# Optimization experiments

Hardware: AMD Instinct MI355X
Metric: run time of the kernel (lower is better)

## Reference

```python
import jax, jax.numpy as jnp
import numpy as np
import math

L, E, H, T, B, V = 6, 768, 12, 1024, 4, 256
HS = E // H


def _ln(x, w, b, eps=1e-5):
    mu = jnp.mean(x, axis=-1, keepdims=True)
    var = jnp.mean((x - mu) ** 2, axis=-1, keepdims=True)
    return (x - mu) * jax.lax.rsqrt(var + eps) * w + b


def setup_inputs() -> dict:
    key = jax.random.key(0)
    ks = jax.random.split(key, 12)
    std = 0.02
    inp = {
        "idx": jax.random.randint(ks[0], (B, T), 0, V, dtype=jnp.int64),
        "tok_emb": jax.random.normal(ks[1], (V, E), jnp.float32) * std,
        "pos_emb": jnp.zeros((1, T, E), jnp.float32),
        "ln1_w": jnp.ones((L, E), jnp.float32),
        "ln1_b": jnp.zeros((L, E), jnp.float32),
        "Wq": jax.random.normal(ks[2], (L, E, E), jnp.float32) * std,
        "bq": jnp.zeros((L, E), jnp.float32),
        "Wk": jax.random.normal(ks[3], (L, E, E), jnp.float32) * std,
        "bk": jnp.zeros((L, E), jnp.float32),
        "Wv": jax.random.normal(ks[4], (L, E, E), jnp.float32) * std,
        "bv": jnp.zeros((L, E), jnp.float32),
        "Wp": jax.random.normal(ks[5], (L, E, E), jnp.float32) * std,
        "bp": jnp.zeros((L, E), jnp.float32),
        "ln2_w": jnp.ones((L, E), jnp.float32),
        "ln2_b": jnp.zeros((L, E), jnp.float32),
        "W1": jax.random.normal(ks[6], (L, E, 4 * E), jnp.float32) * std,
        "b1": jnp.zeros((L, 4 * E), jnp.float32),
        "W2": jax.random.normal(ks[7], (L, 4 * E, E), jnp.float32) * std,
        "b2": jnp.zeros((L, E), jnp.float32),
        "lnf_w": jnp.ones((E,), jnp.float32),
        "lnf_b": jnp.zeros((E,), jnp.float32),
        "lm_head": jax.random.normal(ks[8], (E, V), jnp.float32) * std,
    }
    return inp


def reference(idx, tok_emb, pos_emb, ln1_w, ln1_b, Wq, bq, Wk, bk, Wv, bv, Wp, bp,
              ln2_w, ln2_b, W1, b1, W2, b2, lnf_w, lnf_b, lm_head):
    Bc, Tc = idx.shape
    causal = jnp.tril(jnp.ones((Tc, Tc), bool))  # [T,T]
    scale = 1.0 / math.sqrt(HS)
    x = tok_emb[idx] + pos_emb[:, :Tc, :]  # [B,T,E]
    for l in range(L):
        h = _ln(x, ln1_w[l], ln1_b[l])
        q = (h @ Wq[l] + bq[l]).reshape(Bc, Tc, H, HS).transpose(0, 2, 1, 3)
        k = (h @ Wk[l] + bk[l]).reshape(Bc, Tc, H, HS).transpose(0, 2, 1, 3)
        v = (h @ Wv[l] + bv[l]).reshape(Bc, Tc, H, HS).transpose(0, 2, 1, 3)
        att = jnp.einsum('bhtd,bhsd->bhts', q, k) * scale  # [B,H,T,T]
        att = jnp.where(causal, att, -jnp.inf)
        att = jax.nn.softmax(att, axis=-1)
        y = jnp.einsum('bhts,bhsd->bhtd', att, v)
        y = y.transpose(0, 2, 1, 3).reshape(Bc, Tc, E)
        x = x + (y @ Wp[l] + bp[l])
        h2 = _ln(x, ln2_w[l], ln2_b[l])
        m = jax.nn.gelu(h2 @ W1[l] + b1[l], approximate=False)
        x = x + (m @ W2[l] + b2[l])
    x = _ln(x, lnf_w, lnf_b)
    logits = x @ lm_head  # [B,T,V]
    return logits
```

## Files before the change

kernel.cpp:

```cpp
#include <hip/hip_runtime.h>

#define L_ 6
#define E_ 768
#define H_ 12
#define T_ 1024
#define B_ 4
#define V_ 256
#define M_ (B_*T_)
#define E4_ (4*E_)
#define QKVN (3*E_)
#define NZP 2
#define NZL 4

typedef __bf16 bf16;
typedef __bf16 bf16x8 __attribute__((ext_vector_type(8)));
typedef __bf16 bf16x4 __attribute__((ext_vector_type(4)));
typedef float f32x4 __attribute__((ext_vector_type(4)));

#define GF_GELU     1
#define GF_BIAS_EXT 16
#define GF_PART     32

__device__ __forceinline__ float ldf(const void* p, size_t i, int f32m) {
    return f32m ? ((const float*)p)[i] : (float)((const bf16*)p)[i];
}

__device__ __forceinline__ void async_cp16(const void* g, void* l) {
    __builtin_amdgcn_global_load_lds(
        (__attribute__((address_space(1))) void*)g,
        (__attribute__((address_space(3))) void*)l, 16, 0, 0);
}

__device__ __forceinline__ float exp2_hw(float x) {
    float r; asm("v_exp_f32 %0, %1" : "=v"(r) : "v"(x)); return r;
}

__device__ __forceinline__ float gelu_f(float v) {
    float ax = fabsf(v) * 0.70710678118654752f;
    float t  = 1.f / (1.f + 0.3275911f * ax);
    float p  = t*(0.254829592f + t*(-0.284496736f + t*(1.421413741f
             + t*(-1.453152027f + t*1.061405429f))));
    float e  = exp2_hw(-1.4426950408889634f * ax * ax);
    float er = __builtin_copysignf(1.f - p * e, v);
    return 0.5f * v * (1.f + er);
}

__global__ __launch_bounds__(256) void k_probe(const void* __restrict__ tok,
    const void* __restrict__ idxp, int* __restrict__ dm)
{
    __shared__ int sc1, sc2;
    if (threadIdx.x == 0) { sc1 = 0; sc2 = 0; }
    __syncthreads();
    const bf16* tb = (const bf16*)tok;
    int c1 = 0;
    for (int i = threadIdx.x; i < 4096; i += 256) {
        float v = (float)tb[2 * i];
        if (!(fabsf(v) < 100.f)) c1++;
    }
    const int* ip = (const int*)idxp;
    int c2 = 0;
    for (int i = threadIdx.x; i < 1024; i += 256)
        if (ip[2 * i + 1] != 0) c2++;
    atomicAdd(&sc1, c1);
    atomicAdd(&sc2, c2);
    __syncthreads();
    if (threadIdx.x == 0) { dm[0] = (sc1 > 400) ? 1 : 0; dm[1] = (sc2 < 100) ? 1 : 0; }
}

__global__ __launch_bounds__(256) void k_embed(const void* __restrict__ idxp,
    const void* __restrict__ tok, const void* __restrict__ pos,
    float* __restrict__ x, const int* __restrict__ dm)
{
    int f32m = dm[0], i64m = dm[1];
    int bt = blockIdx.x;
    int t  = bt & (T_ - 1);
    int id = i64m ? ((const int*)idxp)[2 * bt] : ((const int*)idxp)[bt];
    float* xo = x + (size_t)bt * E_;
    for (int e = threadIdx.x; e < E_; e += 256)
        xo[e] = ldf(tok, (size_t)id * E_ + e, f32m) + ldf(pos, (size_t)t * E_ + e, f32m);
}

__global__ __launch_bounds__(256) void k_ln(const float* __restrict__ x,
    const void* __restrict__ w, const void* __restrict__ b, size_t wboff,
    bf16* __restrict__ out, const int* __restrict__ dm)
{
    int f32m = dm[0];
    int row = blockIdx.x;
    int tid = threadIdx.x;
    const float* xr = x + (size_t)row * E_;
    float v0 = xr[tid], v1 = xr[tid + 256], v2 = xr[tid + 512];
    float s  = v0 + v1 + v2;
    float s2 = v0*v0 + v1*v1 + v2*v2;
    for (int off = 32; off; off >>= 1) {
        s  += __shfl_xor(s,  off);
        s2 += __shfl_xor(s2, off);
    }
    __shared__ float ls[4], ls2[4];
    int wave = tid >> 6;
    if ((tid & 63) == 0) { ls[wave] = s; ls2[wave] = s2; }
    __syncthreads();
    s  = ls[0] + ls[1] + ls[2] + ls[3];
    s2 = ls2[0] + ls2[1] + ls2[2] + ls2[3];
    float mu  = s * (1.0f / E_);
    float var = s2 * (1.0f / E_) - mu * mu;
    float rs  = rsqrtf(var + 1e-5f);
    bf16* o = out + (size_t)row * E_;
    o[tid]       = (bf16)(((v0 - mu) * rs) * ldf(w, wboff + tid,       f32m) + ldf(b, wboff + tid,       f32m));
    o[tid + 256] = (bf16)(((v1 - mu) * rs) * ldf(w, wboff + tid + 256, f32m) + ldf(b, wboff + tid + 256, f32m));
    o[tid + 512] = (bf16)(((v2 - mu) * rs) * ldf(w, wboff + tid + 512, f32m) + ldf(b, wboff + tid + 512, f32m));
}

__global__ __launch_bounds__(256) void k_red_ln(float* __restrict__ x,
    const float* __restrict__ part,
    const void* __restrict__ gb, size_t gboff,
    const void* __restrict__ w, const void* __restrict__ b, size_t wboff,
    bf16* __restrict__ out, const int* __restrict__ dm)
{
    const size_t PSTR = (size_t)M_ * E_;
    int f32m = dm[0];
    int row = blockIdx.x;
    int tid = threadIdx.x;
    float* xr = x + (size_t)row * E_;
    const float* pr = part + (size_t)row * E_;
    float v[3];
    #pragma unroll
    for (int j = 0; j < 3; j++) {
        int c = tid + j * 256;
        float acc = xr[c];
        #pragma unroll
        for (int z = 0; z < NZP; z++) acc += pr[(size_t)z * PSTR + c];
        acc += ldf(gb, gboff + c, f32m);
        v[j] = acc;
        xr[c] = acc;
    }
    float s  = v[0] + v[1] + v[2];
    float s2 = v[0]*v[0] + v[1]*v[1] + v[2]*v[2];
    for (int off = 32; off; off >>= 1) {
        s  += __shfl_xor(s,  off);
        s2 += __shfl_xor(s2, off);
    }
    __shared__ float ls[4], ls2[4];
    int wave = tid >> 6;
    if ((tid & 63) == 0) { ls[wave] = s; ls2[wave] = s2; }
    __syncthreads();
    s  = ls[0] + ls[1] + ls[2] + ls[3];
    s2 = ls2[0] + ls2[1] + ls2[2] + ls2[3];
    float mu  = s * (1.0f / E_);
    float var = s2 * (1.0f / E_) - mu * mu;
    float rs  = rsqrtf(var + 1e-5f);
    bf16* o = out + (size_t)row * E_;
    #pragma unroll
    for (int j = 0; j < 3; j++) {
        int c = tid + j * 256;
        o[c] = (bf16)(((v[j] - mu) * rs) * ldf(w, wboff + c, f32m) + ldf(b, wboff + c, f32m));
    }
}

__global__ __launch_bounds__(256) void k_transposeZ(const void* __restrict__ in,
    size_t inoff, size_t zin, bf16* __restrict__ out, size_t zout,
    int R, int C, const int* __restrict__ dm)
{
    int f32m = dm[0];
    __shared__ bf16 tile[32][33];
    size_t io = inoff + (size_t)blockIdx.z * zin;
    bf16* o = out + (size_t)blockIdx.z * zout;
    int r0 = blockIdx.x * 32, c0 = blockIdx.y * 32;
    int tx = threadIdx.x & 31, ty = threadIdx.x >> 5;
    #pragma unroll
    for (int i = 0; i < 4; i++)
        tile[ty + 8*i][tx] = (bf16)ldf(in, io + (size_t)(r0 + ty + 8*i) * C + (c0 + tx), f32m);
    __syncthreads();
    #pragma unroll
    for (int i = 0; i < 4; i++)
        o[(size_t)(c0 + ty + 8*i) * R + (r0 + tx)] = tile[tx][ty + 8*i];
}

__global__ __launch_bounds__(256) void k_transpose3L(const void* __restrict__ a,
    const void* __restrict__ b, const void* __restrict__ c,
    bf16* __restrict__ out, const int* __restrict__ dm)
{
    int f32m = dm[0];
    int z = blockIdx.z, l = z / 3, wsel = z - 3 * l;
    const void* in = (wsel == 0) ? a : ((wsel == 1) ? b : c);
    size_t io = (size_t)l * E_ * E_;
    bf16* o = out + (size_t)z * E_ * E_;
    __shared__ bf16 tile[32][33];
    int r0 = blockIdx.x * 32, c0 = blockIdx.y * 32;
    int tx = threadIdx.x & 31, ty = threadIdx.x >> 5;
    #pragma unroll
    for (int i = 0; i < 4; i++)
        tile[ty + 8*i][tx] = (bf16)ldf(in, io + (size_t)(r0 + ty + 8*i) * E_ + (c0 + tx), f32m);
    __syncthreads();
    #pragma unroll
    for (int i = 0; i < 4; i++)
        o[(size_t)(c0 + ty + 8*i) * E_ + (r0 + tx)] = tile[tx][ty + 8*i];
}

__global__ __launch_bounds__(256) void k_cat3L(const void* __restrict__ a,
    const void* __restrict__ b, const void* __restrict__ c,
    bf16* __restrict__ o, const int* __restrict__ dm)
{
    int f32m = dm[0];
    int i = blockIdx.x * 256 + threadIdx.x;
    int l = i / QKVN, j = i - l * QKVN;
    float v = (j < E_) ? ldf(a, (size_t)l * E_ + j, f32m)
            : ((j < 2*E_) ? ldf(b, (size_t)l * E_ + j - E_, f32m)
                          : ldf(c, (size_t)l * E_ + j - 2*E_, f32m));
    o[i] = (bf16)v;
}

__global__ __launch_bounds__(256) void k_cast_red(const float* __restrict__ in,
    void* __restrict__ out, const int* __restrict__ dm)
{
    const size_t S = (size_t)M_ * V_ / 4;
    size_t i = (size_t)blockIdx.x * 256 + threadIdx.x;
    const f32x4* p = (const f32x4*)in;
    f32x4 v = p[i];
    v += p[S + i];
    v += p[2*S + i];
    v += p[3*S + i];
    if (dm[0]) {
        ((f32x4*)out)[i] = v;
    } else {
        bf16x4 o;
        #pragma unroll
        for (int j = 0; j < 4; j++) o[j] = (bf16)v[j];
        ((bf16x4*)out)[i] = o;
    }
}

__global__ __launch_bounds__(256) void k_gemm(const bf16* __restrict__ A,
    const bf16* __restrict__ BT, const void* __restrict__ bias, size_t boff,
    void* __restrict__ outp, int M, int N, int K, int flags, const int* __restrict__ dm)
{
    int f32m = dm[0];
    __shared__ __attribute__((aligned(16))) bf16 As[128 * 64];
    __shared__ __attribute__((aligned(16))) bf16 Bs[128 * 64];
    int tid = threadIdx.x;
    int bn0 = blockIdx.x * 128, bm0 = blockIdx.y * 128;
    int kz = blockIdx.z;
    int Ks = K / gridDim.z;
    int kbeg = kz * Ks, kend = kbeg + Ks;
    int wave = tid >> 6, lane = tid & 63, quad = lane >> 4, l16 = lane & 15;
    int wr = wave >> 1, wc = wave & 1;

    int st_col = 8 * ((lane & 7) ^ (lane >> 3));
    int st_row_base = wave * 32 + (lane >> 3);

    f32x4 acc[4][4];
    #pragma unroll
    for (int i = 0; i < 4; i++)
        #pragma unroll
        for (int j = 0; j < 4; j++)
            acc[i][j] = (f32x4){0.f, 0.f, 0.f, 0.f};

    int sw = l16 & 7;
    for (int k0 = kbeg; k0 < kend; k0 += 64) {
        #pragma unroll
        for (int i = 0; i < 4; i++) {
            int row = st_row_base + i * 8;
            const bf16* ga = A  + (size_t)(bm0 + row) * K + k0 + st_col;
            const bf16* gb = BT + (size_t)(bn0 + row) * K + k0 + st_col;
            bf16* la = As + (size_t)(wave * 256 + i * 64) * 8;
            bf16* lb = Bs + (size_t)(wave * 256 + i * 64) * 8;
            async_cp16(ga, la);
            async_cp16(gb, lb);
        }
        __syncthreads();
        #pragma unroll
        for (int ks = 0; ks < 2; ks++) {
            bf16x8 af[4], bfr[4];
            #pragma unroll
            for (int mi = 0; mi < 4; mi++) {
                int row = wr*64 + mi*16 + l16;
                int kgs = (4*ks + quad) ^ sw;
                af[mi] = *(const bf16x8*)&As[row*64 + kgs*8];
            }
            #pragma unroll
            for (int ni = 0; ni < 4; ni++) {
                int row = wc*64 + ni*16 + l16;
                int kgs = (4*ks + quad) ^ sw;
                bfr[ni] = *(const bf16x8*)&Bs[row*64 + kgs*8];
            }
            #pragma unroll
            for (int mi = 0; mi < 4; mi++)
                #pragma unroll
                for (int ni = 0; ni < 4; ni++)
                    acc[mi][ni] = __builtin_amdgcn_mfma_f32_16x16x32_bf16(af[mi], bfr[ni], acc[mi][ni], 0, 0, 0);
        }
        __syncthreads();
    }

    float* pout = (float*)outp + (size_t)kz * M * N;
    #pragma unroll
    for (int mi = 0; mi < 4; mi++) {
        #pragma unroll
        for (int ni = 0; ni < 4; ni++) {
            int col = bn0 + wc*64 + ni*16 + l16;
            float bv = 0.f;
            if (bias)
                bv = (flags & GF_BIAS_EXT) ? ldf(bias, boff + col, f32m)
                                           : (float)((const bf16*)bias)[col];
            #pragma unroll
            for (int r = 0; r < 4; r++) {
                int row = bm0 + wr*64 + mi*16 + quad*4 + r;
                float val = acc[mi][ni][r] + bv;
                if (flags & GF_GELU) val = gelu_f(val);
                size_t oidx = (size_t)row * N + col;
                if (flags & GF_PART) pout[oidx] = val;
                else                 ((bf16*)outp)[oidx] = (bf16)val;
            }
        }
    }
}

__global__ __launch_bounds__(256) void k_gemm64(const bf16* __restrict__ A,
    const bf16* __restrict__ BT, void* __restrict__ outp,
    int M, int N, int K, int flags, const int* __restrict__ dm)
{
    __shared__ __attribute__((aligned(16))) bf16 As[128 * 64];
    __shared__ __attribute__((aligned(16))) bf16 Bs[64 * 64];
    int tid = threadIdx.x;
    int bn0 = blockIdx.x * 64, bm0 = blockIdx.y * 128;
    int kz = blockIdx.z;
    int Ks = K / gridDim.z;
    int kbeg = kz * Ks, kend = kbeg + Ks;
    int wave = tid >> 6, lane = tid & 63, quad = lane >> 4, l16 = lane & 15;
    int wr = wave >> 1, wc = wave & 1;

    int st_col = 8 * ((lane & 7) ^ (lane >> 3));
    int lrow = lane >> 3;

    f32x4 acc[4][2];
    #pragma unroll
    for (int i = 0; i < 4; i++)
        #pragma unroll
        for (int j = 0; j < 2; j++)
            acc[i][j] = (f32x4){0.f, 0.f, 0.f, 0.f};

    int sw = l16 & 7;
    for (int k0 = kbeg; k0 < kend; k0 += 64) {
        #pragma unroll
        for (int i = 0; i < 4; i++) {
            int row = wave * 32 + i * 8 + lrow;
            async_cp16(A + (size_t)(bm0 + row) * K + k0 + st_col,
                       As + (size_t)(wave * 32 + i * 8) * 64);
        }
        #pragma unroll
        for (int i = 0; i < 2; i++) {
            int row = wave * 16 + i * 8 + lrow;
            async_cp16(BT + (size_t)(bn0 + row) * K + k0 + st_col,
                       Bs + (size_t)(wave * 16 + i * 8) * 64);
        }
        __syncthreads();
        #pragma unroll
        for (int ks = 0; ks < 2; ks++) {
            int kgs = (4*ks + quad) ^ sw;
            bf16x8 af[4], bfr[2];
            #pragma unroll
            for (int mi = 0; mi < 4; mi++)
                af[mi] = *(const bf16x8*)&As[(wr*64 + mi*16 + l16)*64 + kgs*8];
            #pragma unroll
            for (int ni = 0; ni < 2; ni++)
                bfr[ni] = *(const bf16x8*)&Bs[(wc*32 + ni*16 + l16)*64 + kgs*8];
            #pragma unroll
            for (int mi = 0; mi < 4; mi++)
                #pragma unroll
                for (int ni = 0; ni < 2; ni++)
                    acc[mi][ni] = __builtin_amdgcn_mfma_f32_16x16x32_bf16(af[mi], bfr[ni], acc[mi][ni], 0, 0, 0);
        }
        __syncthreads();
    }

    float* pout = (float*)outp + (size_t)kz * M * N;
    #pragma unroll
    for (int mi = 0; mi < 4; mi++) {
        #pragma unroll
        for (int ni = 0; ni < 2; ni++) {
            int col = bn0 + wc*32 + ni*16 + l16;
            #pragma unroll
            for (int r = 0; r < 4; r++) {
                int row = bm0 + wr*64 + mi*16 + quad*4 + r;
                float val = acc[mi][ni][r];
                size_t oidx = (size_t)row * N + col;
                if (flags & GF_PART) pout[oidx] = val;
                else                 ((bf16*)outp)[oidx] = (bf16)val;
            }
        }
    }
}

__device__ __forceinline__ void attn_qk_softmax2(
    const bf16x8 qf[2], f32x4 OT[4], float& m_ln, float& l_ln,
    const bf16* __restrict__ Kbuf, bf16 (*Ps)[72],
    int wave, int quad, int l16, int s0, int qt0, bool diag)
{
    f32x4 S[4];
    #pragma unroll
    for (int i = 0; i < 4; i++) S[i] = (f32x4){0.f, 0.f, 0.f, 0.f};
    #pragma unroll
    for (int ks = 0; ks < 2; ks++)
        #pragma unroll
        for (int ni = 0; ni < 4; ni++) {
            int kg = (ks*4 + quad) ^ (l16 & 7);
            bf16x8 kf = *(const bf16x8*)&Kbuf[(ni*16 + l16)*64 + kg*8];
            S[ni] = __builtin_amdgcn_mfma_f32_16x16x32_bf16(kf, qf[ks], S[ni], 0, 0, 0);
        }
    const float SC = 0.18033688011112042f;
    if (diag) {
        int qr = qt0 + wave*16 + l16;
        #pragma unroll
        for (int ni = 0; ni < 4; ni++)
            #pragma unroll
            for (int r = 0; r < 4; r++) {
                int scol = s0 + ni*16 + quad*4 + r;
                S[ni][r] = (scol > qr) ? -1e30f : S[ni][r] * SC;
            }
    } else {
        #pragma unroll
        for (int ni = 0; ni < 4; ni++)
            #pragma unroll
            for (int r = 0; r < 4; r++) S[ni][r] *= SC;
    }
    float tn[4];
    #pragma unroll
    for (int ni = 0; ni < 4; ni++)
        tn[ni] = fmaxf(fmaxf(S[ni][0], S[ni][1]), fmaxf(S[ni][2], S[ni][3]));
    float tm = fmaxf(fmaxf(tn[0], tn[1]), fmaxf(tn[2], tn[3]));
    tm = fmaxf(tm, __shfl_xor(tm, 16));
    tm = fmaxf(tm, __shfl_xor(tm, 32));
    float mnew = fmaxf(m_ln, tm);
    float alpha = exp2_hw(m_ln - mnew);
    m_ln = mnew;
    float rsum = 0.f;
    bf16x4 pk[4];
    #pragma unroll
    for (int ni = 0; ni < 4; ni++)
        #pragma unroll
        for (int r = 0; r < 4; r++) {
            float p = exp2_hw(S[ni][r] - mnew);
            rsum += p;
            pk[ni][r] = (bf16)p;
        }
    rsum += __shfl_xor(rsum, 16);
    rsum += __shfl_xor(rsum, 32);
    l_ln = l_ln * alpha + rsum;
    #pragma unroll
    for (int ni = 0; ni < 4; ni++)
        #pragma unroll
        for (int r = 0; r < 4; r++) OT[ni][r] *= alpha;
    #pragma unroll
    for (int ni = 0; ni < 4; ni++)
        *(bf16x4*)&Ps[wave*16 + l16][ni*16 + quad*4] = pk[ni];
}

__device__ __forceinline__ void attn_pv(
    f32x4 OT[4], const bf16 (*Ps)[72], const bf16 (*Vt)[72],
    int wave, int quad, int l16)
{
    #pragma unroll
    for (int ks = 0; ks < 2; ks++) {
        bf16x8 pf = *(const bf16x8*)&Ps[wave*16 + l16][ks*32 + quad*8];
        #pragma unroll
        for (int ni = 0; ni < 4; ni++) {
            bf16x8 vf = *(const bf16x8*)&Vt[ni*16 + l16][ks*32 + quad*8];
            OT[ni] = __builtin_amdgcn_mfma_f32_16x16x32_bf16(vf, pf, OT[ni], 0, 0, 0);
        }
    }
}

__global__ __launch_bounds__(256) void k_attn(const bf16* __restrict__ qkv, bf16* __restrict__ y)
{
    int x = blockIdx.x;
    int qt = x * 64;
    int h = blockIdx.y, b = blockIdx.z;
    int tid = threadIdx.x, wave = tid >> 6, lane = tid & 63, quad = lane >> 4, l16 = lane & 15;

    const bf16* qb = qkv + (size_t)b * T_ * QKVN + h * 64;
    const bf16* kb = qb + E_;
    const bf16* vb = qb + 2 * E_;

    __shared__ __attribute__((aligned(16))) bf16 Kbuf[64 * 64];
    __shared__ __attribute__((aligned(16))) bf16 Vbuf[64 * 64];
    __shared__ __attribute__((aligned(16))) bf16 Vt[64][72];
    __shared__ __attribute__((aligned(16))) bf16 Ps[64][72];

    int srow = tid >> 3;
    int scol = 8 * ((lane & 7) ^ (srow & 7));

    bf16x8 qf[2];
    {
        int qr = qt + wave * 16 + l16;
        #pragma unroll
        for (int ks = 0; ks < 2; ks++)
            qf[ks] = *(const bf16x8*)(qb + (size_t)qr * QKVN + ks*32 + quad*8);
    }

    f32x4 OT[4];
    #pragma unroll
    for (int i = 0; i < 4; i++) OT[i] = (f32x4){0.f,0.f,0.f,0.f};
    float m_ln = -3.0e38f, l_ln = 0.f;

    auto stage = [&](int s0) {
        #pragma unroll
        for (int i = 0; i < 2; i++) {
            int row = i * 32 + srow;
            const bf16* gk = kb + (size_t)(s0 + row) * QKVN + scol;
            const bf16* gv = vb + (size_t)(s0 + row) * QKVN + scol;
            bf16* lk = Kbuf + ((size_t)i * 32 + wave * 8) * 64;
            bf16* lv = Vbuf + ((size_t)i * 32 + wave * 8) * 64;
            async_cp16(gk, lk);
            async_cp16(gv, lv);
        }
    };

    stage(0);
    asm volatile("s_waitcnt vmcnt(0)" ::: "memory");
    __syncthreads();

    for (int st = 0; st <= x; st++) {
        int s0 = st * 64;
        {
            int d = lane;
            int dg = d >> 3, de = d & 7;
            #pragma unroll
            for (int ii = 0; ii < 2; ii++) {
                int sb = wave * 2 + ii;
                bf16x8 tv;
                #pragma unroll
                for (int j = 0; j < 8; j++)
                    tv[j] = Vbuf[(sb*8 + j) * 64 + ((dg ^ j) * 8) + de];
                *(bf16x8*)&Vt[d][sb * 8] = tv;
            }
        }
        attn_qk_softmax2(qf, OT, m_ln, l_ln, Kbuf, Ps, wave, quad, l16, s0, qt, st == x);
        __syncthreads();
        if (st < x) stage(s0 + 64);
        attn_pv(OT, Ps, Vt, wave, quad, l16);
        asm volatile("s_waitcnt vmcnt(0)" ::: "memory");
        __syncthreads();
    }

    float inv = 1.f / l_ln;
    int qrow = qt + wave * 16 + l16;
    #pragma unroll
    for (int ni = 0; ni < 4; ni++) {
        bf16x4 ov;
        #pragma unroll
        for (int r = 0; r < 4; r++) ov[r] = (bf16)(OT[ni][r] * inv);
        *(bf16x4*)&y[(size_t)(b * T_ + qrow) * E_ + h*64 + ni*16 + quad*4] = ov;
    }
}

extern "C" void kernel_launch(void* const* d_in, const int* in_sizes, int n_in,
                              void* d_out, int out_size, void* d_ws, size_t ws_size,
                              hipStream_t stream)
{
    const void* idx     = d_in[0];
    const void* tok_emb = d_in[1];
    const void* pos_emb = d_in[2];
    const void* ln1_w   = d_in[3];
    const void* ln1_b   = d_in[4];
    const void* Wq      = d_in[5];
    const void* bq      = d_in[6];
    const void* Wk      = d_in[7];
    const void* bk      = d_in[8];
    const void* Wv      = d_in[9];
    const void* bv      = d_in[10];
    const void* Wp      = d_in[11];
    const void* bp      = d_in[12];
    const void* ln2_w   = d_in[13];
    const void* ln2_b   = d_in[14];
    const void* W1      = d_in[15];
    const void* b1      = d_in[16];
    const void* W2      = d_in[17];
    const void* b2      = d_in[18];
    const void* lnf_w   = d_in[19];
    const void* lnf_b   = d_in[20];
    const void* lm_head = d_in[21];

    char* base = (char*)d_ws;
    size_t off = 0;
    auto nxt = [&](size_t bytes) -> void* {
        void* p = base + off;
        off += (bytes + 255) & ~(size_t)255;
        return p;
    };
    int*   dm    = (int*)  nxt(256);
    float* x     = (float*)nxt((size_t)M_ * E_ * 4);
    bf16*  h     = (bf16*) nxt((size_t)M_ * E_ * 2);
    bf16*  qkv   = (bf16*) nxt((size_t)M_ * QKVN * 2);
    bf16*  yb    = (bf16*) nxt((size_t)M_ * E_ * 2);
    bf16*  mbuf  = (bf16*) nxt((size_t)M_ * E4_ * 2);
    bf16*  wqkvT = (bf16*) nxt((size_t)L_ * 3 * E_ * E_ * 2);
    bf16*  wpT   = (bf16*) nxt((size_t)L_ * E_ * E_ * 2);
    bf16*  w1T   = (bf16*) nxt((size_t)L_ * E_ * E4_ * 2);
    bf16*  w2T   = (bf16*) nxt((size_t)L_ * E4_ * E_ * 2);
    bf16*  lmhT  = (bf16*) nxt((size_t)V_ * E_ * 2);
    bf16*  bcat  = (bf16*) nxt((size_t)L_ * QKVN * 2);
    float* part  = (float*)nxt((size_t)NZL * M_ * V_ * 4 > (size_t)NZP * M_ * E_ * 4
                             ? (size_t)NZL * M_ * V_ * 4 : (size_t)NZP * M_ * E_ * 4);
    (void)ws_size; (void)in_sizes; (void)n_in; (void)out_size;

    k_probe<<<1, 256, 0, stream>>>(tok_emb, idx, dm);
    k_embed<<<M_, 256, 0, stream>>>(idx, tok_emb, pos_emb, x, dm);

    k_transpose3L<<<dim3(E_/32, E_/32, 3*L_), 256, 0, stream>>>(Wq, Wk, Wv, wqkvT, dm);
    k_transposeZ<<<dim3(E_/32, E_/32, L_), 256, 0, stream>>>(Wp, 0, (size_t)E_*E_, wpT, (size_t)E_*E_, E_, E_, dm);
    k_transposeZ<<<dim3(E_/32, E4_/32, L_), 256, 0, stream>>>(W1, 0, (size_t)E_*E4_, w1T, (size_t)E_*E4_, E_, E4_, dm);
    k_transposeZ<<<dim3(E4_/32, E_/32, L_), 256, 0, stream>>>(W2, 0, (size_t)E_*E4_, w2T, (size_t)E_*E4_, E4_, E_, dm);
    k_transposeZ<<<dim3(E_/32, V_/32, 1), 256, 0, stream>>>(lm_head, 0, 0, lmhT, 0, E_, V_, dm);
    k_cat3L<<<(L_*QKVN)/256, 256, 0, stream>>>(bq, bk, bv, bcat, dm);

    k_ln<<<M_, 256, 0, stream>>>(x, ln1_w, ln1_b, 0, h, dm);

    for (int l = 0; l < L_; l++) {
        size_t voE  = (size_t)l * E_;
        size_t voE4 = (size_t)l * E4_;

        k_gemm<<<dim3(QKVN/128, M_/128), 256, 0, stream>>>(h, wqkvT + (size_t)l*3*E_*E_,
            bcat + (size_t)l*QKVN, 0, qkv, M_, QKVN, E_, 0, dm);

        k_attn<<<dim3(16, H_, B_), 256, 0, stream>>>(qkv, yb);

        k_gemm64<<<dim3(E_/64, M_/128, NZP), 256, 0, stream>>>(yb, wpT + (size_t)l*E_*E_,
            part, M_, E_, E_, GF_PART, dm);
        k_red_ln<<<M_, 256, 0, stream>>>(x, part, bp, voE, ln2_w, ln2_b, voE, h, dm);

        k_gemm<<<dim3(E4_/128, M_/128), 256, 0, stream>>>(h, w1T + (size_t)l*E_*E4_,
            b1, voE4, mbuf, M_, E4_, E_, GF_GELU | GF_BIAS_EXT, dm);

        k_gemm64<<<dim3(E_/64, M_/128, NZP), 256, 0, stream>>>(mbuf, w2T + (size_t)l*E_*E4_,
            part, M_, E_, E4_, GF_PART, dm);
        if (l < L_ - 1)
            k_red_ln<<<M_, 256, 0, stream>>>(x, part, b2, voE, ln1_w, ln1_b, (size_t)(l+1) * E_, h, dm);
        else
            k_red_ln<<<M_, 256, 0, stream>>>(x, part, b2, voE, lnf_w, lnf_b, 0, h, dm);
    }

    k_gemm64<<<dim3(V_/64, M_/128, NZL), 256, 0, stream>>>(h, lmhT, part, M_, V_, E_, GF_PART, dm);
    k_cast_red<<<(M_*V_)/1024, 256, 0, stream>>>(part, d_out, dm);
}
```

Before: 1.366 ms.

## Double-buffer GEMM LDS tiles and fuse residual add into projection epilogues

Both GEMM kernels now keep two LDS buffers and issue the async global-to-LDS copy for the next K tile while computing on the current one, so load latency can overlap with MFMA work. The projection and FC2 GEMMs no longer split K into fp32 partial buffers. They add bias and accumulate directly into the fp32 residual x in the epilogue, which lets the partial-sum reduction kernel be replaced by a plain LayerNorm. In exchange, LDS use doubles, which may reduce occupancy, and the K=768 projection GEMM loses the parallelism that split-K gave it (only 384 blocks). Only one barrier remains per iteration, and it is unclear whether the async LDS writes are waited on before they are read.

```diff
diff --git a/kernel.cpp b/kernel.cpp
--- a/kernel.cpp
+++ b/kernel.cpp
@@ -9,7 +9,6 @@
 #define M_ (B_*T_)
 #define E4_ (4*E_)
 #define QKVN (3*E_)
-#define NZP 2
 #define NZL 4
 
 typedef __bf16 bf16;
@@ -20,6 +19,7 @@
 #define GF_GELU     1
 #define GF_BIAS_EXT 16
 #define GF_PART     32
+#define GF_RESID    64
 
 __device__ __forceinline__ float ldf(const void* p, size_t i, int f32m) {
     return f32m ? ((const float*)p)[i] : (float)((const bf16*)p)[i];
@@ -108,52 +108,6 @@
     o[tid]       = (bf16)(((v0 - mu) * rs) * ldf(w, wboff + tid,       f32m) + ldf(b, wboff + tid,       f32m));
     o[tid + 256] = (bf16)(((v1 - mu) * rs) * ldf(w, wboff + tid + 256, f32m) + ldf(b, wboff + tid + 256, f32m));
     o[tid + 512] = (bf16)(((v2 - mu) * rs) * ldf(w, wboff + tid + 512, f32m) + ldf(b, wboff + tid + 512, f32m));
-}
-
-__global__ __launch_bounds__(256) void k_red_ln(float* __restrict__ x,
-    const float* __restrict__ part,
-    const void* __restrict__ gb, size_t gboff,
-    const void* __restrict__ w, const void* __restrict__ b, size_t wboff,
-    bf16* __restrict__ out, const int* __restrict__ dm)
-{
-    const size_t PSTR = (size_t)M_ * E_;
-    int f32m = dm[0];
-    int row = blockIdx.x;
-    int tid = threadIdx.x;
-    float* xr = x + (size_t)row * E_;
-    const float* pr = part + (size_t)row * E_;
-    float v[3];
-    #pragma unroll
-    for (int j = 0; j < 3; j++) {
-        int c = tid + j * 256;
-        float acc = xr[c];
-        #pragma unroll
-        for (int z = 0; z < NZP; z++) acc += pr[(size_t)z * PSTR + c];
-        acc += ldf(gb, gboff + c, f32m);
-        v[j] = acc;
-        xr[c] = acc;
-    }
-    float s  = v[0] + v[1] + v[2];
-    float s2 = v[0]*v[0] + v[1]*v[1] + v[2]*v[2];
-    for (int off = 32; off; off >>= 1) {
-        s  += __shfl_xor(s,  off);
-        s2 += __shfl_xor(s2, off);
-    }
-    __shared__ float ls[4], ls2[4];
-    int wave = tid >> 6;
-    if ((tid & 63) == 0) { ls[wave] = s; ls2[wave] = s2; }
-    __syncthreads();
-    s  = ls[0] + ls[1] + ls[2] + ls[3];
-    s2 = ls2[0] + ls2[1] + ls2[2] + ls2[3];
-    float mu  = s * (1.0f / E_);
-    float var = s2 * (1.0f / E_) - mu * mu;
-    float rs  = rsqrtf(var + 1e-5f);
-    bf16* o = out + (size_t)row * E_;
-    #pragma unroll
-    for (int j = 0; j < 3; j++) {
-        int c = tid + j * 256;
-        o[c] = (bf16)(((v[j] - mu) * rs) * ldf(w, wboff + c, f32m) + ldf(b, wboff + c, f32m));
-    }
 }
 
 __global__ __launch_bounds__(256) void k_transposeZ(const void* __restrict__ in,
@@ -234,13 +188,10 @@
     void* __restrict__ outp, int M, int N, int K, int flags, const int* __restrict__ dm)
 {
     int f32m = dm[0];
-    __shared__ __attribute__((aligned(16))) bf16 As[128 * 64];
-    __shared__ __attribute__((aligned(16))) bf16 Bs[128 * 64];
+    __shared__ __attribute__((aligned(16))) bf16 As[2][128 * 64];
+    __shared__ __attribute__((aligned(16))) bf16 Bs[2][128 * 64];
     int tid = threadIdx.x;
     int bn0 = blockIdx.x * 128, bm0 = blockIdx.y * 128;
-    int kz = blockIdx.z;
-    int Ks = K / gridDim.z;
-    int kbeg = kz * Ks, kend = kbeg + Ks;
     int wave = tid >> 6, lane = tid & 63, quad = lane >> 4, l16 = lane & 15;
     int wr = wave >> 1, wc = wave & 1;
 
@@ -254,34 +205,34 @@
         for (int j = 0; j < 4; j++)
             acc[i][j] = (f32x4){0.f, 0.f, 0.f, 0.f};
 
-    int sw = l16 & 7;
-    for (int k0 = kbeg; k0 < kend; k0 += 64) {
+    auto stage = [&](int buf, int k0) {
         #pragma unroll
         for (int i = 0; i < 4; i++) {
             int row = st_row_base + i * 8;
-            const bf16* ga = A  + (size_t)(bm0 + row) * K + k0 + st_col;
-            const bf16* gb = BT + (size_t)(bn0 + row) * K + k0 + st_col;
-            bf16* la = As + (size_t)(wave * 256 + i * 64) * 8;
-            bf16* lb = Bs + (size_t)(wave * 256 + i * 64) * 8;
-            async_cp16(ga, la);
-            async_cp16(gb, lb);
-        }
-        __syncthreads();
+            async_cp16(A  + (size_t)(bm0 + row) * K + k0 + st_col,
+                       &As[buf][(wave * 256 + i * 64) * 8]);
+            async_cp16(BT + (size_t)(bn0 + row) * K + k0 + st_col,
+                       &Bs[buf][(wave * 256 + i * 64) * 8]);
+        }
+    };
+
+    int nt = K / 64;
+    int sw = l16 & 7;
+    stage(0, 0);
+    __syncthreads();
+    for (int t = 0; t < nt; ++t) {
+        int cur = t & 1;
+        if (t + 1 < nt) stage(cur ^ 1, (t + 1) * 64);
         #pragma unroll
         for (int ks = 0; ks < 2; ks++) {
             bf16x8 af[4], bfr[4];
-            #pragma unroll
-            for (int mi = 0; mi < 4; mi++) {
-                int row = wr*64 + mi*16 + l16;
-                int kgs = (4*ks + quad) ^ sw;
-                af[mi] = *(const bf16x8*)&As[row*64 + kgs*8];
-            }
-            #pragma unroll
-            for (int ni = 0; ni < 4; ni++) {
-                int row = wc*64 + ni*16 + l16;
-                int kgs = (4*ks + quad) ^ sw;
-                bfr[ni] = *(const bf16x8*)&Bs[row*64 + kgs*8];
-            }
+            int kgs = (4*ks + quad) ^ sw;
+            #pragma unroll
+            for (int mi = 0; mi < 4; mi++)
+                af[mi] = *(const bf16x8*)&As[cur][(wr*64 + mi*16 + l16)*64 + kgs*8];
+            #pragma unroll
+            for (int ni = 0; ni < 4; ni++)
+                bfr[ni] = *(const bf16x8*)&Bs[cur][(wc*64 + ni*16 + l16)*64 + kgs*8];
             #pragma unroll
             for (int mi = 0; mi < 4; mi++)
                 #pragma unroll
@@ -291,7 +242,6 @@
         __syncthreads();
     }
 
-    float* pout = (float*)outp + (size_t)kz * M * N;
     #pragma unroll
     for (int mi = 0; mi < 4; mi++) {
         #pragma unroll
@@ -307,24 +257,24 @@
                 float val = acc[mi][ni][r] + bv;
                 if (flags & GF_GELU) val = gelu_f(val);
                 size_t oidx = (size_t)row * N + col;
-                if (flags & GF_PART) pout[oidx] = val;
-                else                 ((bf16*)outp)[oidx] = (bf16)val;
+                ((bf16*)outp)[oidx] = (bf16)val;
             }
         }
     }
 }
 
 __global__ __launch_bounds__(256) void k_gemm64(const bf16* __restrict__ A,
-    const bf16* __restrict__ BT, void* __restrict__ outp,
-    int M, int N, int K, int flags, const int* __restrict__ dm)
-{
-    __shared__ __attribute__((aligned(16))) bf16 As[128 * 64];
-    __shared__ __attribute__((aligned(16))) bf16 Bs[64 * 64];
+    const bf16* __restrict__ BT, const void* __restrict__ bias, size_t boff,
+    void* __restrict__ outp, int M, int N, int K, int flags, const int* __restrict__ dm)
+{
+    int f32m = dm[0];
+    __shared__ __attribute__((aligned(16))) bf16 As[2][128 * 64];
+    __shared__ __attribute__((aligned(16))) bf16 Bs[2][64 * 64];
     int tid = threadIdx.x;
     int bn0 = blockIdx.x * 64, bm0 = blockIdx.y * 128;
     int kz = blockIdx.z;
     int Ks = K / gridDim.z;
-    int kbeg = kz * Ks, kend = kbeg + Ks;
+    int kbeg = kz * Ks;
     int wave = tid >> 6, lane = tid & 63, quad = lane >> 4, l16 = lane & 15;
     int wr = wave >> 1, wc = wave & 1;
 
@@ -338,31 +288,38 @@
         for (int j = 0; j < 2; j++)
             acc[i][j] = (f32x4){0.f, 0.f, 0.f, 0.f};
 
-    int sw = l16 & 7;
-    for (int k0 = kbeg; k0 < kend; k0 += 64) {
+    auto stage = [&](int buf, int k0) {
         #pragma unroll
         for (int i = 0; i < 4; i++) {
             int row = wave * 32 + i * 8 + lrow;
             async_cp16(A + (size_t)(bm0 + row) * K + k0 + st_col,
-                       As + (size_t)(wave * 32 + i * 8) * 64);
+                       &As[buf][(size_t)(wave * 32 + i * 8) * 64]);
         }
         #pragma unroll
         for (int i = 0; i < 2; i++) {
             int row = wave * 16 + i * 8 + lrow;
             async_cp16(BT + (size_t)(bn0 + row) * K + k0 + st_col,
-                       Bs + (size_t)(wave * 16 + i * 8) * 64);
-        }
-        __syncthreads();
+                       &Bs[buf][(size_t)(wave * 16 + i * 8) * 64]);
+        }
+    };
+
+    int nt = Ks / 64;
+    int sw = l16 & 7;
+    stage(0, kbeg);
+    __syncthreads();
+    for (int t = 0; t < nt; ++t) {
+        int cur = t & 1;
+        if (t + 1 < nt) stage(cur ^ 1, kbeg + (t + 1) * 64);
         #pragma unroll
         for (int ks = 0; ks < 2; ks++) {
             int kgs = (4*ks + quad) ^ sw;
             bf16x8 af[4], bfr[2];
             #pragma unroll
             for (int mi = 0; mi < 4; mi++)
-                af[mi] = *(const bf16x8*)&As[(wr*64 + mi*16 + l16)*64 + kgs*8];
+                af[mi] = *(const bf16x8*)&As[cur][(wr*64 + mi*16 + l16)*64 + kgs*8];
             #pragma unroll
             for (int ni = 0; ni < 2; ni++)
-                bfr[ni] = *(const bf16x8*)&Bs[(wc*32 + ni*16 + l16)*64 + kgs*8];
+                bfr[ni] = *(const bf16x8*)&Bs[cur][(wc*32 + ni*16 + l16)*64 + kgs*8];
             #pragma unroll
             for (int mi = 0; mi < 4; mi++)
                 #pragma unroll
@@ -378,13 +335,23 @@
         #pragma unroll
         for (int ni = 0; ni < 2; ni++) {
             int col = bn0 + wc*32 + ni*16 + l16;
+            float bv = 0.f;
+            if (bias)
+                bv = (flags & GF_BIAS_EXT) ? ldf(bias, boff + col, f32m)
+                                           : (float)((const bf16*)bias)[col];
             #pragma unroll
             for (int r = 0; r < 4; r++) {
                 int row = bm0 + wr*64 + mi*16 + quad*4 + r;
-                float val = acc[mi][ni][r];
+                float val = acc[mi][ni][r] + bv;
                 size_t oidx = (size_t)row * N + col;
-                if (flags & GF_PART) pout[oidx] = val;
-                else                 ((bf16*)outp)[oidx] = (bf16)val;
+                if (flags & GF_RESID) {
+                    float* xo = (float*)outp;
+                    xo[oidx] += val;
+                } else if (flags & GF_PART) {
+                    pout[oidx] = val;
+                } else {
+                    ((bf16*)outp)[oidx] = (bf16)val;
+                }
             }
         }
     }
@@ -598,8 +565,7 @@
     bf16*  w2T   = (bf16*) nxt((size_t)L_ * E4_ * E_ * 2);
     bf16*  lmhT  = (bf16*) nxt((size_t)V_ * E_ * 2);
     bf16*  bcat  = (bf16*) nxt((size_t)L_ * QKVN * 2);
-    float* part  = (float*)nxt((size_t)NZL * M_ * V_ * 4 > (size_t)NZP * M_ * E_ * 4
-                             ? (size_t)NZL * M_ * V_ * 4 : (size_t)NZP * M_ * E_ * 4);
+    float* part  = (float*)nxt((size_t)NZL * M_ * V_ * 4);
     (void)ws_size; (void)in_sizes; (void)n_in; (void)out_size;
 
     k_probe<<<1, 256, 0, stream>>>(tok_emb, idx, dm);
@@ -623,21 +589,22 @@
 
         k_attn<<<dim3(16, H_, B_), 256, 0, stream>>>(qkv, yb);
 
-        k_gemm64<<<dim3(E_/64, M_/128, NZP), 256, 0, stream>>>(yb, wpT + (size_t)l*E_*E_,
-            part, M_, E_, E_, GF_PART, dm);
-        k_red_ln<<<M_, 256, 0, stream>>>(x, part, bp, voE, ln2_w, ln2_b, voE, h, dm);
+        k_gemm64<<<dim3(E_/64, M_/128), 256, 0, stream>>>(yb, wpT + (size_t)l*E_*E_,
+            bp, voE, x, M_, E_, E_, GF_RESID | GF_BIAS_EXT, dm);
+        k_ln<<<M_, 256, 0, stream>>>(x, ln2_w, ln2_b, voE, h, dm);
 
         k_gemm<<<dim3(E4_/128, M_/128), 256, 0, stream>>>(h, w1T + (size_t)l*E_*E4_,
             b1, voE4, mbuf, M_, E4_, E_, GF_GELU | GF_BIAS_EXT, dm);
 
-        k_gemm64<<<dim3(E_/64, M_/128, NZP), 256, 0, stream>>>(mbuf, w2T + (size_t)l*E_*E4_,
-            part, M_, E_, E4_, GF_PART, dm);
+        k_gemm64<<<dim3(E_/64, M_/128), 256, 0, stream>>>(mbuf, w2T + (size_t)l*E_*E4_,
+            b2, voE, x, M_, E_, E4_, GF_RESID | GF_BIAS_EXT, dm);
         if (l < L_ - 1)
-            k_red_ln<<<M_, 256, 0, stream>>>(x, part, b2, voE, ln1_w, ln1_b, (size_t)(l+1) * E_, h, dm);
+            k_ln<<<M_, 256, 0, stream>>>(x, ln1_w, ln1_b, (size_t)(l+1) * E_, h, dm);
         else
-            k_red_ln<<<M_, 256, 0, stream>>>(x, part, b2, voE, lnf_w, lnf_b, 0, h, dm);
-    }
-
-    k_gemm64<<<dim3(V_/64, M_/128, NZL), 256, 0, stream>>>(h, lmhT, part, M_, V_, E_, GF_PART, dm);
+            k_ln<<<M_, 256, 0, stream>>>(x, lnf_w, lnf_b, 0, h, dm);
+    }
+
+    k_gemm64<<<dim3(V_/64, M_/128, NZL), 256, 0, stream>>>(h, lmhT, nullptr, 0,
+        part, M_, V_, E_, GF_PART, dm);
     k_cast_red<<<(M_*V_)/1024, 256, 0, stream>>>(part, d_out, dm);
 }
```

After: 1.524 ms. +11.6%, slower.
